# Kernel optimization log

Measured on AMD Instinct MI355X. Metric: run time of the kernel, lower is better.

## Reference

```python
import jax, jax.numpy as jnp
import numpy as np

HIDDEN, KEY_DIM, VALUE_DIM = 1024, 1024, 1024
BATCH, SEQ = 8, 2048


def setup_inputs() -> dict:
    key = jax.random.key(0)
    ks = jax.random.split(key, 9)
    s = lambda fan_in: 1.0 / np.sqrt(fan_in)
    return {
        "y_all": jax.random.normal(ks[0], (BATCH, SEQ, HIDDEN), dtype=jnp.float32),
        # torch nn.Linear weights stored as (in, out) for x @ W + b
        "Wq": jax.random.uniform(ks[1], (HIDDEN, KEY_DIM), jnp.float32, -s(HIDDEN), s(HIDDEN)),
        "bq": jax.random.uniform(ks[2], (KEY_DIM,), jnp.float32, -s(HIDDEN), s(HIDDEN)),
        "Wk": jax.random.uniform(ks[3], (HIDDEN, KEY_DIM), jnp.float32, -s(HIDDEN), s(HIDDEN)),
        "bk": jax.random.uniform(ks[4], (KEY_DIM,), jnp.float32, -s(HIDDEN), s(HIDDEN)),
        "Wv": jax.random.uniform(ks[5], (HIDDEN, VALUE_DIM), jnp.float32, -s(HIDDEN), s(HIDDEN)),
        "bv": jax.random.uniform(ks[6], (VALUE_DIM,), jnp.float32, -s(HIDDEN), s(HIDDEN)),
        "Wo": jax.random.uniform(ks[7], (VALUE_DIM, HIDDEN), jnp.float32, -s(VALUE_DIM), s(VALUE_DIM)),
        "bo": jax.random.uniform(ks[8], (HIDDEN,), jnp.float32, -s(VALUE_DIM), s(VALUE_DIM)),
    }


def reference(y_all, Wq, bq, Wk, bk, Wv, bv, Wo, bo):
    # Original loops over t, each step attending last hidden state to the full
    # prefix. Equivalent to a single causal-masked attention pass.
    B, T, H = y_all.shape
    dk = Wq.shape[1]
    q = (y_all @ Wq + bq) / jnp.sqrt(jnp.asarray(dk, y_all.dtype))  # [B,T,dk]
    k = y_all @ Wk + bk                                              # [B,T,dk]
    v = y_all @ Wv + bv                                              # [B,T,dv]
    scores = jnp.einsum("bid,bjd->bij", q, k)                        # [B,T,T]
    causal = jnp.tril(jnp.ones((T, T), dtype=bool))                  # j <= i
    scores = jnp.where(causal, scores, -jnp.inf)
    weights = jax.nn.softmax(scores, axis=-1)
    ctx = jnp.einsum("bij,bjd->bid", weights, v)                     # [B,T,dv]
    return ctx @ Wo + bo                                             # [B,T,H]
```

## Files before the change

### kernel.cpp

```cpp
#include <hip/hip_runtime.h>

typedef __attribute__((ext_vector_type(8))) __bf16 bf16x8;
typedef __attribute__((ext_vector_type(4))) float f32x4;
typedef __attribute__((ext_vector_type(4))) float f4;
typedef __attribute__((ext_vector_type(4))) unsigned short ushort4_t;

__device__ inline void gload16(const void* g, void* l) {
  __builtin_amdgcn_global_load_lds(
      (const __attribute__((address_space(1))) unsigned int*)g,
      (__attribute__((address_space(3))) unsigned int*)l, 16, 0, 0);
}

__global__ void convert_bf16_k(const float* __restrict__ in, __bf16* __restrict__ out, int n8) {
  int i = blockIdx.x * blockDim.x + threadIdx.x;
  int stride = gridDim.x * blockDim.x;
  for (; i < n8; i += stride) {
    f4 a = ((const f4*)in)[2 * (long long)i];
    f4 b = ((const f4*)in)[2 * (long long)i + 1];
    bf16x8 o;
#pragma unroll
    for (int e = 0; e < 4; e++) { o[e] = (__bf16)a[e]; o[e + 4] = (__bf16)b[e]; }
    ((bf16x8*)out)[i] = o;
  }
}

__global__ void pack_bias_k(const float* __restrict__ bq, const float* __restrict__ bk,
                            const float* __restrict__ bv, float* __restrict__ out) {
  int i = blockIdx.x * 256 + threadIdx.x;
  if (i >= 3072) return;
  const float* src = (i < 1024) ? bq : (i < 2048) ? bk : bv;
  out[i] = src[i & 1023];
}

__global__ void transpose_w_k(const float* __restrict__ W0, const float* __restrict__ W1,
                              const float* __restrict__ W2, const float* __restrict__ W3,
                              __bf16* __restrict__ out) {
  int z = blockIdx.z;
  const float* W = (z == 0) ? W0 : (z == 1) ? W1 : (z == 2) ? W2 : W3;
  __bf16* O = out + (long long)z * 1048576;
  __shared__ float tile[32][33];
  int tx = threadIdx.x, ty = threadIdx.y;
  int n0 = blockIdx.x * 32, k0 = blockIdx.y * 32;
#pragma unroll
  for (int i = 0; i < 4; i++)
    tile[ty + i * 8][tx] = W[(long long)(k0 + ty + i * 8) * 1024 + n0 + tx];
  __syncthreads();
#pragma unroll
  for (int i = 0; i < 4; i++)
    O[(long long)(n0 + ty + i * 8) * 1024 + k0 + tx] = (__bf16)tile[tx][ty + i * 8];
}


#define LOADA(BASE, MIB)                                                       \
  _Pragma("unroll") for (int mi = 0; mi < 4; mi++)                             \
      _Pragma("unroll") for (int kh = 0; kh < 2; kh++) {                       \
    int row = ((MIB) + mi) * 16 + ln15;                                        \
    int pb = (row * 128 + (kh * 32 + kq * 8) * 2) ^ ((row & 7) << 4);          \
    a[mi][kh] = *(const bf16x8*)((BASE) + pb);                                 \
  }

#define LOADB(BASE, NIB)                                                       \
  _Pragma("unroll") for (int ni = 0; ni < 2; ni++)                             \
      _Pragma("unroll") for (int kh = 0; kh < 2; kh++) {                       \
    int row = brow0 + ((NIB) + ni) * 16 + ln15;                                \
    int pb = (row * 128 + (kh * 32 + kq * 8) * 2) ^ ((row & 7) << 4);          \
    b[(NIB) + ni][kh] = *(const bf16x8*)((BASE) + pb);                         \
  }

#define MFMAQ(MI0, NI0)                                                        \
  _Pragma("unroll") for (int mi = 0; mi < 4; mi++)                             \
      _Pragma("unroll") for (int ni = 0; ni < 2; ni++)                         \
          _Pragma("unroll") for (int kh = 0; kh < 2; kh++)                     \
              acc[(MI0) + mi][(NI0) + ni] =                                    \
      __builtin_amdgcn_mfma_f32_16x16x32_bf16(a[mi][kh], b[(NI0) + ni][kh],    \
                                              acc[(MI0) + mi][(NI0) + ni], 0, 0, 0);

#define FENCE asm volatile("" ::: "memory")

#define BARW                                           \
  FENCE;                                               \
  __builtin_amdgcn_s_barrier();                        \
  FENCE;                                               \
  __builtin_amdgcn_s_setprio(1);

#define ENDP                                           \
  __builtin_amdgcn_s_setprio(0);                       \
  FENCE;                                               \
  __builtin_amdgcn_s_barrier();                        \
  FENCE;

#define ENDPB                                          \
  __builtin_amdgcn_s_setprio(0);                       \
  asm volatile("s_waitcnt vmcnt(8)" ::: "memory");     \
  __builtin_amdgcn_s_barrier();                        \
  FENCE;

template <int OUT, int SWZ>
__global__ __launch_bounds__(512, 2) void gemm8(
    const __bf16* __restrict__ A0, int lda, long long sAz,
    const __bf16* __restrict__ B0, int ldb, long long sBz,
    void* __restrict__ C0v, int ldc, long long sCz,
    const float* __restrict__ bias0, int sBiasZ,
    float scale_z0, int k_tiles_base, int k_tiles_per_br,
    __bf16* __restrict__ vt_out) {
  int br, bc, z;
  {
    const int lin = (blockIdx.z * gridDim.y + blockIdx.y) * gridDim.x + blockIdx.x;
    if (SWZ == 2) {
      const int q = lin & 7, c = lin >> 3;
      z = q;
      int b0 = (int)((sqrtf((float)(8 * c + 1)) - 1.0f) * 0.5f);
      int c0 = c - ((b0 * (b0 + 1)) >> 1);
      if (c0 < 0) { b0--; c0 = c - ((b0 * (b0 + 1)) >> 1); }
      if (c0 > b0) { b0++; c0 = c - ((b0 * (b0 + 1)) >> 1); }
      br = b0;
      bc = c0;
    } else if (SWZ == 3) {
      const int q = lin & 7, c = lin >> 3;
      z = q;
      br = c & 7;
      bc = c >> 3;
    } else {
      const int nbx = gridDim.x, nby = gridDim.y;
      const int nwg = nbx * nby * gridDim.z;
      const int cpx = nwg >> 3;
      const int swz = (lin & 7) * cpx + (lin >> 3);
      br = swz % nbx;
      const int tmp = swz / nbx;
      bc = tmp % nby;
      z = tmp / nby;
    }
  }
  const int kt = k_tiles_base + k_tiles_per_br * br;

  __shared__ __align__(16) __bf16 lds[81920];

  const int t = threadIdx.x, w = t >> 6, lane = t & 63;
  const int wm = w >> 2, wn = w & 3;
  const int ln15 = lane & 15, kq = lane >> 4;
  const int bh = wn >> 1, brow0 = (wn & 1) * 64;

  const __bf16* A = A0 + (long long)z * sAz + (long long)br * 256 * lda;
  const __bf16* B = B0 + (long long)z * sBz + (long long)bc * 256 * ldb;

  int r0s[2], c0s[2];
#pragma unroll
  for (int i = 0; i < 2; i++) {
    int o = i * 8192 + t * 16;
    int lo = o ^ (((o >> 7) & 7) << 4);
    r0s[i] = lo >> 7;
    c0s[i] = (lo & 127) >> 1;
  }
  const __bf16 *sA0[2], *sA1[2], *sB0[2], *sB1[2];
#pragma unroll
  for (int i = 0; i < 2; i++) {
    sA0[i] = A + (long long)r0s[i] * lda + c0s[i];
    sA1[i] = A + (long long)(r0s[i] + 128) * lda + c0s[i];
    sB0[i] = B + (long long)r0s[i] * ldb + c0s[i];
    sB1[i] = B + (long long)(r0s[i] + 128) * ldb + c0s[i];
  }

  auto stg = [&](const __bf16* const* src, __bf16* lbase, int g) {
    int kc = g < kt ? g : kt - 1;
#pragma unroll
    for (int i = 0; i < 2; i++)
      gload16(src[i] + kc * 64, lbase + i * 4096 + w * 512);
  };

  f32x4 acc[8][4] = {};
  bf16x8 a[4][2], b[4][2];

  stg(sA0, lds, 0);
  stg(sA1, lds + 8192, 0);
  stg(sB0, lds + 49152, 0);
  stg(sB1, lds + 49152 + 8192, 0);
  stg(sA0, lds + 16384, 1);
  stg(sA1, lds + 16384 + 8192, 1);
  stg(sB0, lds + 65536, 1);
  stg(sB1, lds + 65536 + 8192, 1);
  asm volatile("s_waitcnt vmcnt(8)" ::: "memory");
  __builtin_amdgcn_s_barrier();
  FENCE;

  int ap = 0;
  int ad = 2;
  for (int kk = 0; kk < kt; kk++) {
    __bf16* Ab = lds + ap * 16384;
    __bf16* Bb = lds + 49152 + (kk & 1) * 16384;
    __bf16* Ad = lds + ad * 16384;
    __bf16* Bd = Bb;
    const char* Aw = (const char*)(Ab + wm * 8192);
    const char* Bw = (const char*)(Bb + bh * 8192);
    LOADA(Aw, 0) LOADB(Bw, 0)
    stg(sA0, Ad, kk + 2);
    BARW MFMAQ(0, 0) ENDP
    LOADB(Bw, 2)
    stg(sA1, Ad + 8192, kk + 2);
    BARW MFMAQ(0, 2) ENDP
    LOADA(Aw, 4)
    stg(sB0, Bd, kk + 2);
    BARW MFMAQ(4, 2) ENDP
    stg(sB1, Bd + 8192, kk + 2);
    BARW MFMAQ(4, 0) ENDPB
    ap = (ap == 2) ? 0 : ap + 1;
    ad = (ad == 2) ? 0 : ad + 1;
  }

  if (OUT == 2 && z == 2) {
    __syncthreads();
    char* lb = (char*)lds;
    const int dl0 = wn * 64 + ln15;
    const int tl0 = wm * 128 + kq * 4;
#pragma unroll
    for (int mi = 0; mi < 8; mi++) {
#pragma unroll
      for (int ni = 0; ni < 4; ni++) {
        const int d = dl0 + ni * 16;
        const int tl = tl0 + mi * 16;
        const float bb = bias0[2048 + bc * 256 + d];
        ushort4_t p;
#pragma unroll
        for (int j = 0; j < 4; j++) {
          union { __bf16 h; unsigned short u; } cv;
          cv.h = (__bf16)(acc[mi][ni][j] + bb);
          p[j] = cv.u;
        }
        int byte = d * 512 + tl * 2;
        byte ^= (d & 7) << 4;
        *(ushort4_t*)(lb + byte) = p;
      }
    }
    __syncthreads();
    const int bz = br >> 3;
    __bf16* vbase = vt_out + (long long)bz * 2097152 +
                    (long long)(bc * 256) * 2048 + (br & 7) * 256;
#pragma unroll
    for (int it = 0; it < 16; it++) {
      int idx = it * 512 + t;
      int d = idx >> 5, tc = idx & 31;
      int byte = d * 512 + tc * 16;
      byte ^= (d & 7) << 4;
      bf16x8 vv = *(const bf16x8*)(lb + byte);
      *(bf16x8*)(vbase + (long long)d * 2048 + tc * 8) = vv;
    }
  } else {
    const int row0 = br * 256 + wm * 128 + kq * 4;
    const int col0 = bc * 256 + wn * 64 + ln15;
    const float scale = (z == 0) ? scale_z0 : 1.0f;
    const float* bias = bias0 ? (bias0 + (long long)z * sBiasZ) : nullptr;
#pragma unroll
    for (int mi = 0; mi < 8; mi++) {
#pragma unroll
      for (int ni = 0; ni < 4; ni++) {
        const int rr = row0 + mi * 16;
        const int cc = col0 + ni * 16;
        const float bb = bias ? bias[cc] : 0.0f;
#pragma unroll
        for (int j = 0; j < 4; j++) {
          float v = (acc[mi][ni][j] + bb) * scale;
          long long off = (long long)z * sCz + (long long)(rr + j) * ldc + cc;
          if (OUT == 1)
            ((float*)C0v)[off] = v;
          else
            ((__bf16*)C0v)[off] = (__bf16)v;
        }
      }
    }
  }
}

__global__ __launch_bounds__(256) void softmax_rows(__bf16* __restrict__ S) {
  const int row = blockIdx.x;
  const int i = row & 2047;
  __bf16* s = S + (long long)row * 2048;
  const int Lpad = (i + 256) & ~255;
  const int t = threadIdx.x;
  const int j0 = t * 8;
  const int wid = t >> 6, lane = t & 63;
  const bool active = j0 < Lpad;

  float v[8];
  float mymax = -3.0e38f;
  if (active) {
    bf16x8 x = *(const bf16x8*)(s + j0);
#pragma unroll
    for (int e = 0; e < 8; e++) {
      float f = (float)x[e];
      v[e] = ((j0 + e) <= i) ? f : -3.0e38f;
      mymax = fmaxf(mymax, v[e]);
    }
  }
  float mw = mymax;
#pragma unroll
  for (int o = 32; o >= 1; o >>= 1) mw = fmaxf(mw, __shfl_xor(mw, o));
  __shared__ float redm[4];
  __shared__ float reds[4];
  if (lane == 0) redm[wid] = mw;
  __syncthreads();
  const float m = fmaxf(fmaxf(redm[0], redm[1]), fmaxf(redm[2], redm[3]));

  float e8[8];
  float mysum = 0.0f;
  if (active) {
#pragma unroll
    for (int e = 0; e < 8; e++) {
      float ev = ((j0 + e) <= i) ? __expf(v[e] - m) : 0.0f;
      e8[e] = ev;
      mysum += ev;
    }
  } else {
#pragma unroll
    for (int e = 0; e < 8; e++) e8[e] = 0.0f;
  }
  float sw = mysum;
#pragma unroll
  for (int o = 32; o >= 1; o >>= 1) sw += __shfl_xor(sw, o);
  if (lane == 0) reds[wid] = sw;
  __syncthreads();
  const float l = reds[0] + reds[1] + reds[2] + reds[3];
  const float rl = 1.0f / l;
  if (active) {
    bf16x8 o;
#pragma unroll
    for (int e = 0; e < 8; e++) o[e] = (__bf16)(e8[e] * rl);
    *(bf16x8*)(s + j0) = o;
  }
}

extern "C" void kernel_launch(void* const* d_in, const int* in_sizes, int n_in,
                              void* d_out, int out_size, void* d_ws, size_t ws_size,
                              hipStream_t stream) {
  const float* y  = (const float*)d_in[0];
  const float* Wq = (const float*)d_in[1];
  const float* bq = (const float*)d_in[2];
  const float* Wk = (const float*)d_in[3];
  const float* bk = (const float*)d_in[4];
  const float* Wv = (const float*)d_in[5];
  const float* bv = (const float*)d_in[6];
  const float* Wo = (const float*)d_in[7];
  const float* bo = (const float*)d_in[8];

  char* ws = (char*)d_ws;
  __bf16* Xb   = (__bf16*)(ws + 0);
  __bf16* Wt   = (__bf16*)(ws + 33554432);
  float*  bqkv = (float*)(ws + 41943040);
  __bf16* Qb   = (__bf16*)(ws + 41955328);
  __bf16* Kb   = (__bf16*)(ws + 75509760);
  __bf16* Vt   = (__bf16*)(ws + 109064192);
  __bf16* Sb   = (__bf16*)(ws + 142618624);
  __bf16* ctx  = (__bf16*)(ws + 0);

  if (ws_size < 209727488u) return;

  convert_bf16_k<<<2048, 256, 0, stream>>>(y, Xb, 2097152);
  pack_bias_k<<<12, 256, 0, stream>>>(bq, bk, bv, bqkv);
  transpose_w_k<<<dim3(32, 32, 4), dim3(32, 8), 0, stream>>>(Wq, Wk, Wv, Wo, Wt);

  gemm8<2, 0><<<dim3(64, 4, 3), 512, 0, stream>>>(
      Xb, 1024, 0LL, Wt, 1024, 1048576LL,
      Qb, 1024, 16777216LL, bqkv, 1024, 0.03125f, 16, 0, Vt);

  gemm8<0, 2><<<dim3(36, 1, 8), 512, 0, stream>>>(
      Qb, 1024, 2097152LL, Kb, 1024, 2097152LL,
      Sb, 2048, 4194304LL, nullptr, 0, 1.0f, 16, 0, nullptr);

  softmax_rows<<<16384, 256, 0, stream>>>(Sb);

  gemm8<0, 3><<<dim3(8, 4, 8), 512, 0, stream>>>(
      Sb, 2048, 4194304LL, Vt, 2048, 2097152LL,
      ctx, 1024, 2097152LL, nullptr, 0, 1.0f, 4, 4, nullptr);

  gemm8<1, 0><<<dim3(64, 4, 1), 512, 0, stream>>>(
      ctx, 1024, 0LL, Wt + 3 * 1048576, 1024, 0LL,
      d_out, 1024, 0LL, bo, 0, 1.0f, 16, 0, nullptr);
}
```

Before: 334.4 us.

## Add 128x256 tile GEMM kernel for QKV and output projections

Introduces a new gemm2w kernel with 128x256 output tiles, a K-step of 32, triple-buffered LDS and higher occupancy (launch bounds 512,4). It replaces the 256x256 gemm8 for the QKV projection, including the transposed V write, and for the output projection. The grid doubles along M and each block uses less LDS, aiming for more resident blocks and better latency hiding. The trade-off is less data reuse per block and more barriers per unit of work. The V-transpose epilogue is removed from gemm8.

```diff
diff --git a/kernel.cpp b/kernel.cpp
--- a/kernel.cpp
+++ b/kernel.cpp
@@ -50,6 +50,8 @@
     O[(long long)(n0 + ty + i * 8) * 1024 + k0 + tx] = (__bf16)tile[tx][ty + i * 8];
 }
 
+#define FENCE asm volatile("" ::: "memory")
+
 
 #define LOADA(BASE, MIB)                                                       \
   _Pragma("unroll") for (int mi = 0; mi < 4; mi++)                             \
@@ -74,8 +76,6 @@
               acc[(MI0) + mi][(NI0) + ni] =                                    \
       __builtin_amdgcn_mfma_f32_16x16x32_bf16(a[mi][kh], b[(NI0) + ni][kh],    \
                                               acc[(MI0) + mi][(NI0) + ni], 0, 0, 0);
-
-#define FENCE asm volatile("" ::: "memory")
 
 #define BARW                                           \
   FENCE;                                               \
@@ -182,8 +182,7 @@
   __builtin_amdgcn_s_barrier();
   FENCE;
 
-  int ap = 0;
-  int ad = 2;
+  int ap = 0, ad = 2;
   for (int kk = 0; kk < kt; kk++) {
     __bf16* Ab = lds + ap * 16384;
     __bf16* Bb = lds + 49152 + (kk & 1) * 16384;
@@ -206,17 +205,140 @@
     ad = (ad == 2) ? 0 : ad + 1;
   }
 
+  {
+    const int row0 = br * 256 + wm * 128 + kq * 4;
+    const int col0 = bc * 256 + wn * 64 + ln15;
+    const float scale = (z == 0) ? scale_z0 : 1.0f;
+    const float* bias = bias0 ? (bias0 + (long long)z * sBiasZ) : nullptr;
+#pragma unroll
+    for (int mi = 0; mi < 8; mi++) {
+#pragma unroll
+      for (int ni = 0; ni < 4; ni++) {
+        const int rr = row0 + mi * 16;
+        const int cc = col0 + ni * 16;
+        const float bb = bias ? bias[cc] : 0.0f;
+#pragma unroll
+        for (int j = 0; j < 4; j++) {
+          float v = (acc[mi][ni][j] + bb) * scale;
+          long long off = (long long)z * sCz + (long long)(rr + j) * ldc + cc;
+          if (OUT == 1)
+            ((float*)C0v)[off] = v;
+          else
+            ((__bf16*)C0v)[off] = (__bf16)v;
+        }
+      }
+    }
+  }
+  (void)vt_out;
+}
+
+template <int OUT>
+__global__ __launch_bounds__(512, 4) void gemm2w(
+    const __bf16* __restrict__ A0, int lda, long long sAz,
+    const __bf16* __restrict__ B0, int ldb, long long sBz,
+    void* __restrict__ C0v, int ldc, long long sCz,
+    const float* __restrict__ bias0, int sBiasZ,
+    float scale_z0, int kt, __bf16* __restrict__ vt_out) {
+  int br, bc, z;
+  {
+    const int lin = (blockIdx.z * gridDim.y + blockIdx.y) * gridDim.x + blockIdx.x;
+    const int q = lin & 7, c = lin >> 3;
+    br = q * 16 + (c & 15);
+    const int rest = c >> 4;
+    const int nby = gridDim.y;
+    bc = rest % nby;
+    z = rest / nby;
+  }
+
+  __shared__ __align__(16) __bf16 lds[36864];
+
+  const int t = threadIdx.x, w = t >> 6, lane = t & 63;
+  const int wm = w >> 2, wn = w & 3;
+  const int ln15 = lane & 15, kq = lane >> 4;
+
+  const __bf16* A = A0 + (long long)z * sAz + (long long)br * 128 * lda;
+  const __bf16* B = B0 + (long long)z * sBz + (long long)bc * 256 * ldb;
+
+  const __bf16* sA;
+  const __bf16* sB[2];
+  {
+    int o = t * 16;
+    int lo = o ^ (((o >> 6) & 3) << 4);
+    sA = A + (long long)(lo >> 6) * lda + ((lo & 63) >> 1);
+  }
+#pragma unroll
+  for (int i = 0; i < 2; i++) {
+    int o = i * 8192 + t * 16;
+    int lo = o ^ (((o >> 6) & 3) << 4);
+    sB[i] = B + (long long)(lo >> 6) * ldb + ((lo & 63) >> 1);
+  }
+
+  auto stgA = [&](int buf, int g) {
+    int kc = g < kt ? g : kt - 1;
+    gload16(sA + kc * 32, lds + buf * 4096 + w * 512);
+  };
+  auto stgB = [&](int buf, int g) {
+    int kc = g < kt ? g : kt - 1;
+#pragma unroll
+    for (int i = 0; i < 2; i++)
+      gload16(sB[i] + kc * 32, lds + 12288 + buf * 8192 + i * 4096 + w * 512);
+  };
+
+  f32x4 acc[4][4] = {};
+  bf16x8 a[4], b[4];
+
+  stgA(0, 0); stgB(0, 0);
+  stgA(1, 1); stgB(1, 1);
+  asm volatile("s_waitcnt vmcnt(3)" ::: "memory");
+  __builtin_amdgcn_s_barrier();
+  FENCE;
+
+  int cb = 0, db = 2;
+  for (int kk = 0; kk < kt; kk++) {
+    const char* Ab = (const char*)(lds + cb * 4096);
+    const char* Bb = (const char*)(lds + 12288 + cb * 8192);
+#pragma unroll
+    for (int mi = 0; mi < 4; mi++) {
+      int row = wm * 64 + mi * 16 + ln15;
+      int pb = (row * 64 + kq * 16) ^ ((row & 3) << 4);
+      a[mi] = *(const bf16x8*)(Ab + pb);
+    }
+#pragma unroll
+    for (int ni = 0; ni < 4; ni++) {
+      int row = wn * 64 + ni * 16 + ln15;
+      int pb = (row * 64 + kq * 16) ^ ((row & 3) << 4);
+      b[ni] = *(const bf16x8*)(Bb + pb);
+    }
+    stgA(db, kk + 2);
+    stgB(db, kk + 2);
+    FENCE;
+    __builtin_amdgcn_s_barrier();
+    FENCE;
+    __builtin_amdgcn_s_setprio(1);
+#pragma unroll
+    for (int mi = 0; mi < 4; mi++)
+#pragma unroll
+      for (int ni = 0; ni < 4; ni++)
+        acc[mi][ni] = __builtin_amdgcn_mfma_f32_16x16x32_bf16(
+            a[mi], b[ni], acc[mi][ni], 0, 0, 0);
+    __builtin_amdgcn_s_setprio(0);
+    asm volatile("s_waitcnt vmcnt(3)" ::: "memory");
+    __builtin_amdgcn_s_barrier();
+    FENCE;
+    cb = (cb == 2) ? 0 : cb + 1;
+    db = (db == 2) ? 0 : db + 1;
+  }
+  asm volatile("s_waitcnt vmcnt(0)" ::: "memory");
+
   if (OUT == 2 && z == 2) {
     __syncthreads();
     char* lb = (char*)lds;
-    const int dl0 = wn * 64 + ln15;
-    const int tl0 = wm * 128 + kq * 4;
-#pragma unroll
-    for (int mi = 0; mi < 8; mi++) {
+#pragma unroll
+    for (int mi = 0; mi < 4; mi++) {
 #pragma unroll
       for (int ni = 0; ni < 4; ni++) {
-        const int d = dl0 + ni * 16;
-        const int tl = tl0 + mi * 16;
+        const int d = wn * 64 + ni * 16 + ln15;
+        const int tl = wm * 64 + kq * 4 + mi * 16;
         const float bb = bias0[2048 + bc * 256 + d];
         ushort4_t p;
 #pragma unroll
@@ -225,31 +347,30 @@
           cv.h = (__bf16)(acc[mi][ni][j] + bb);
           p[j] = cv.u;
         }
-        int byte = d * 512 + tl * 2;
-        byte ^= (d & 7) << 4;
+        int byte = (d * 256 + tl * 2) ^ ((d & 3) << 4);
         *(ushort4_t*)(lb + byte) = p;
       }
     }
     __syncthreads();
-    const int bz = br >> 3;
+    const int bz = br >> 4;
+    const int t0 = (br & 15) * 128;
     __bf16* vbase = vt_out + (long long)bz * 2097152 +
-                    (long long)(bc * 256) * 2048 + (br & 7) * 256;
-#pragma unroll
-    for (int it = 0; it < 16; it++) {
+                    (long long)(bc * 256) * 2048 + t0;
+#pragma unroll
+    for (int it = 0; it < 8; it++) {
       int idx = it * 512 + t;
-      int d = idx >> 5, tc = idx & 31;
-      int byte = d * 512 + tc * 16;
-      byte ^= (d & 7) << 4;
+      int d = idx >> 4, tc = idx & 15;
+      int byte = (d * 256 + tc * 16) ^ ((d & 3) << 4);
       bf16x8 vv = *(const bf16x8*)(lb + byte);
       *(bf16x8*)(vbase + (long long)d * 2048 + tc * 8) = vv;
     }
   } else {
-    const int row0 = br * 256 + wm * 128 + kq * 4;
+    const int row0 = br * 128 + wm * 64 + kq * 4;
     const int col0 = bc * 256 + wn * 64 + ln15;
     const float scale = (z == 0) ? scale_z0 : 1.0f;
     const float* bias = bias0 ? (bias0 + (long long)z * sBiasZ) : nullptr;
 #pragma unroll
-    for (int mi = 0; mi < 8; mi++) {
+    for (int mi = 0; mi < 4; mi++) {
 #pragma unroll
       for (int ni = 0; ni < 4; ni++) {
         const int rr = row0 + mi * 16;
@@ -356,9 +477,9 @@
   pack_bias_k<<<12, 256, 0, stream>>>(bq, bk, bv, bqkv);
   transpose_w_k<<<dim3(32, 32, 4), dim3(32, 8), 0, stream>>>(Wq, Wk, Wv, Wo, Wt);
 
-  gemm8<2, 0><<<dim3(64, 4, 3), 512, 0, stream>>>(
+  gemm2w<2><<<dim3(128, 4, 3), 512, 0, stream>>>(
       Xb, 1024, 0LL, Wt, 1024, 1048576LL,
-      Qb, 1024, 16777216LL, bqkv, 1024, 0.03125f, 16, 0, Vt);
+      Qb, 1024, 16777216LL, bqkv, 1024, 0.03125f, 32, Vt);
 
   gemm8<0, 2><<<dim3(36, 1, 8), 512, 0, stream>>>(
       Qb, 1024, 2097152LL, Kb, 1024, 2097152LL,
@@ -370,7 +491,7 @@
       Sb, 2048, 4194304LL, Vt, 2048, 2097152LL,
       ctx, 1024, 2097152LL, nullptr, 0, 1.0f, 4, 4, nullptr);
 
-  gemm8<1, 0><<<dim3(64, 4, 1), 512, 0, stream>>>(
+  gemm2w<1><<<dim3(128, 4, 1), 512, 0, stream>>>(
       ctx, 1024, 0LL, Wt + 3 * 1048576, 1024, 0LL,
-      d_out, 1024, 0LL, bo, 0, 1.0f, 16, 0, nullptr);
-}
+      d_out, 1024, 0LL, bo, 0, 1.0f, 32, nullptr);
+}
```

Result: no change. 332.7 us (-0.5%).
